# Performance work log

Measured on AMD Instinct MI355X. Metric: run time of the kernel, lower is better.

The kernel has to match this reference:

```python
import jax, jax.numpy as jnp
import numpy as np

B, N, C = 4096, 20, 512
S_VIEWS = 8
N_VIEWS = 20


def setup_inputs() -> dict:
    key = jax.random.key(0)
    k1, k2, k3, k4 = jax.random.split(key, 4)
    F0 = jax.random.normal(k1, (B, N, C), dtype=jnp.float32)
    vertices0 = jax.random.normal(k2, (B, N, 3), dtype=jnp.float32)
    W1 = jax.random.normal(k3, (C, 256), dtype=jnp.float32) * 0.04
    b1 = jnp.zeros((256,), dtype=jnp.float32)
    W2 = jax.random.normal(k4, (256, 40), dtype=jnp.float32) * 0.06
    b2 = jnp.zeros((40,), dtype=jnp.float32)
    return {"F0": F0, "vertices0": vertices0, "W1": W1, "b1": b1, "W2": W2, "b2": b2, "k": 8}


def _cls(x, W1, b1, W2, b2):
    # Linear(512,256) -> LeakyReLU(0.2) -> Linear(256,40)
    h = x @ W1 + b1
    h = jnp.where(h > 0, h, 0.2 * h)
    return h @ W2 + b2


def reference(F0, vertices0, W1, b1, W2, b2, k):
    # F0: [B, N, C]; vertices0: [B, N, 3]
    pooled_F = jnp.sum(F0, axis=1) / N_VIEWS                 # [B, C]
    pred = jnp.argmax(_cls(pooled_F, W1, b1, W2, b2), -1)    # [B] predicted class per sample
    score = _cls(F0, W1, b1, W2, b2)                         # [B, N, 40]
    # score[arange(B), :, pred] -> per-view score of the predicted class
    score_F = jnp.take_along_axis(score, pred[:, None, None], axis=2)[..., 0]  # [B, N]
    _, idx = jax.lax.top_k(score_F, S_VIEWS)                 # [B, S]
    F_new = jnp.take_along_axis(F0, idx[:, :, None], axis=1)            # [B, S, C]
    vertices_new = jnp.take_along_axis(vertices0, idx[:, :, None], axis=1)  # [B, S, 3]
    return (F_new, score, vertices_new)
```

## Files before the change

kernel.cpp:

```cpp
#include <hip/hip_runtime.h>
#include <cstdint>

#define BB 4096
#define NV 20
#define CC 512
#define HH 256
#define NC 40
#define SV 8
#define GG 3
#define TAU 2e-4f

typedef short short8 __attribute__((ext_vector_type(8)));
typedef float f32x4 __attribute__((ext_vector_type(4)));
typedef unsigned short ushort4v __attribute__((ext_vector_type(4)));

__device__ __forceinline__ unsigned short f2bf(float x) {
    unsigned u = __float_as_uint(x);
    unsigned r = (u + 0x7FFFu + ((u >> 16) & 1u)) >> 16;
    return (unsigned short)r;
}
__device__ __forceinline__ float bf2f(unsigned short h) {
    return __uint_as_float(((unsigned)h) << 16);
}

#define MFMA16(A, B, C) __builtin_amdgcn_mfma_f32_16x16x32_bf16(A, B, C, 0, 0, 0)
#define BC8(x) __builtin_bit_cast(short8, x)

__global__ void w1pack_kernel(const float* __restrict__ W1,
                              unsigned short* __restrict__ w1fh,
                              unsigned short* __restrict__ w1fl) {
    int e = blockIdx.x * 256 + threadIdx.x;
    int j3 = e & 7, kq = (e >> 3) & 3, n = (e >> 5) & 255, ks = e >> 13;
    int k = ks * 32 + kq * 8 + j3;
    float x = W1[k * HH + n];
    unsigned short h = f2bf(x);
    w1fh[e] = h;
    w1fl[e] = f2bf(x - bf2f(h));
}

__global__ void w2pack_kernel(const float* __restrict__ W2,
                              unsigned short* __restrict__ w2fh,
                              unsigned short* __restrict__ w2fl) {
    int e = blockIdx.x * 256 + threadIdx.x;
    int j3 = e & 7, kq = (e >> 3) & 3;
    int t = e >> 5;
    int n = t % 48, ks = t / 48;
    int k = ks * 32 + kq * 8 + j3;
    float x = (n < NC) ? W2[k * NC + n] : 0.f;
    unsigned short h = f2bf(x);
    w2fh[e] = h;
    w2fl[e] = f2bf(x - bf2f(h));
}

__global__ __launch_bounds__(256, 3) void fused_kernel(
    const float* __restrict__ F0, const float* __restrict__ V0,
    const float* __restrict__ W1, const float* __restrict__ b1,
    const float* __restrict__ W2, const float* __restrict__ b2,
    const unsigned short* __restrict__ w1fh, const unsigned short* __restrict__ w1fl,
    const unsigned short* __restrict__ w2fh, const unsigned short* __restrict__ w2fl,
    float* __restrict__ outF, float* __restrict__ outS, float* __restrict__ outV)
{
    const int blk = blockIdx.x;
    const int j = threadIdx.x;
    const int L = j & 63, wq = j >> 6, l15 = L & 15, kq = L >> 4;

    __shared__ __align__(16) char lds[51040];
    __shared__ int idx8[GG][SV];
    __shared__ int flags0[GG], flags1[GG], predS[GG];
    __shared__ double part[NV][4];
    __shared__ double SFdS[NV];

    unsigned short* Ahi0 = (unsigned short*)lds;
    unsigned short* Alo0 = Ahi0 + 64 * 72;
    unsigned short* Ahi1 = (unsigned short*)(lds + 18432);
    unsigned short* Alo1 = Ahi1 + 64 * 72;
    unsigned short* Hhi  = (unsigned short*)lds;
    unsigned short* Hlo  = Hhi + 32 * 264;
    float*  Sc      = (float*)(lds + 40960);
    double* pooledD = (double*)lds;
    double* Dbuf    = (double*)(lds + 4096);
    double* Sd      = (double*)(lds + 6144);
    float*  Xf      = (float*)lds;

    f32x4 acc[4][4];
#pragma unroll
    for (int mt = 0; mt < 4; ++mt)
#pragma unroll
        for (int nt = 0; nt < 4; ++nt) acc[mt][nt] = (f32x4){0.f, 0.f, 0.f, 0.f};

    const float4* srcp[4];
    int ldst[4];
    bool sval[4];
#pragma unroll
    for (int i = 0; i < 4; ++i) {
        int f = j + 256 * i;
        int row = f >> 4, k4 = f & 15;
        sval[i] = (row < 60);
        int bi = (row >= 40) ? 2 : (row >= 20) ? 1 : 0;
        int r = row - 20 * bi;
        int batch = blk * GG + bi; if (batch > BB - 1) batch = BB - 1;
        srcp[i] = (const float4*)(F0 + ((size_t)batch * NV + r) * CC) + k4;
        ldst[i] = row * 72 + k4 * 4;
    }

    float4 rv[4];
    auto STAGE_LOAD = [&](int kc) {
#pragma unroll
        for (int i = 0; i < 4; ++i)
            if (sval[i]) rv[i] = srcp[i][kc * 16];
    };
    auto STAGE_CONVERT = [&](unsigned short* __restrict__ Ah,
                             unsigned short* __restrict__ Al) {
#pragma unroll
        for (int i = 0; i < 4; ++i) {
            ushort4v hv = {0, 0, 0, 0}, lv = {0, 0, 0, 0};
            if (sval[i]) {
                float4 x = rv[i];
                hv.x = f2bf(x.x); lv.x = f2bf(x.x - bf2f(hv.x));
                hv.y = f2bf(x.y); lv.y = f2bf(x.y - bf2f(hv.y));
                hv.z = f2bf(x.z); lv.z = f2bf(x.z - bf2f(hv.z));
                hv.w = f2bf(x.w); lv.w = f2bf(x.w - bf2f(hv.w));
            }
            *(ushort4v*)&Ah[ldst[i]] = hv;
            *(ushort4v*)&Al[ldst[i]] = lv;
        }
    };

    const uint4* Bh = (const uint4*)w1fh;
    const uint4* Bl = (const uint4*)w1fl;

    STAGE_LOAD(0);
    STAGE_CONVERT(Ahi0, Alo0);
    STAGE_LOAD(1);
    __syncthreads();

    unsigned short *Ahc = Ahi0, *Alc = Alo0, *Ahn = Ahi1, *Aln = Alo1;
    for (int kc = 0; kc < 8; ++kc) {
        if (kc < 7) {
            STAGE_CONVERT(Ahn, Aln);
            if (kc < 6) STAGE_LOAD(kc + 2);
        }
#pragma unroll
        for (int ks_l = 0; ks_l < 2; ++ks_l) {
            int ks = kc * 2 + ks_l;
            uint4 bh[4], bl[4];
#pragma unroll
            for (int nt = 0; nt < 4; ++nt) {
                int bi1 = (ks * 256 + wq * 64 + nt * 16 + l15) * 4 + kq;
                bh[nt] = Bh[bi1]; bl[nt] = Bl[bi1];
            }
#pragma unroll
            for (int mt = 0; mt < 4; ++mt) {
                int off = (mt * 16 + l15) * 72 + ks_l * 32 + kq * 8;
                short8 Ah = BC8(*(const uint4*)&Ahc[off]);
                short8 Al = BC8(*(const uint4*)&Alc[off]);
#pragma unroll
                for (int nt = 0; nt < 4; ++nt) {
                    short8 Bhv = BC8(bh[nt]), Blv = BC8(bl[nt]);
                    acc[mt][nt] = MFMA16(Ah, Bhv, acc[mt][nt]);
                    acc[mt][nt] = MFMA16(Ah, Blv, acc[mt][nt]);
                    acc[mt][nt] = MFMA16(Al, Bhv, acc[mt][nt]);
                }
            }
        }
        __syncthreads();
        unsigned short* t;
        t = Ahc; Ahc = Ahn; Ahn = t;
        t = Alc; Alc = Aln; Aln = t;
    }

    const uint4* B2h = (const uint4*)w2fh;
    const uint4* B2l = (const uint4*)w2fl;
#pragma unroll
    for (int p = 0; p < 2; ++p) {
        __syncthreads();
#pragma unroll
        for (int mt2 = 0; mt2 < 2; ++mt2) {
            int mt = 2 * p + mt2;
            bool skip = (p == 1 && mt2 == 1 && kq == 3);
#pragma unroll
            for (int nt = 0; nt < 4; ++nt) {
                int col = wq * 64 + nt * 16 + l15;
                float bc = b1[col];
#pragma unroll
                for (int reg = 0; reg < 4; ++reg) {
                    int hb = mt2 * 16 + kq * 4 + reg;
                    float h = acc[mt][nt][reg] + bc;
                    h = (h > 0.f) ? h : 0.2f * h;
                    if (!skip) {
                        unsigned short hh = f2bf(h);
                        Hhi[hb * 264 + col] = hh;
                        Hlo[hb * 264 + col] = f2bf(h - bf2f(hh));
                    }
                }
            }
        }
        if (p == 1) {
#pragma unroll
            for (int nt = 0; nt < 4; ++nt) {
                int col = wq * 64 + nt * 16 + l15;
                float p0 = 0.f, p1 = 0.f, p2 = 0.f;
#pragma unroll
                for (int mt = 0; mt < 4; ++mt)
#pragma unroll
                    for (int reg = 0; reg < 4; ++reg) {
                        int g = mt * 16 + kq * 4 + reg;
                        float v = acc[mt][nt][reg];
                        p0 += (g < 20) ? v : 0.f;
                        p1 += (g >= 20 && g < 40) ? v : 0.f;
                        p2 += (g >= 40 && g < 60) ? v : 0.f;
                    }
                p0 += __shfl_xor(p0, 16); p0 += __shfl_xor(p0, 32);
                p1 += __shfl_xor(p1, 16); p1 += __shfl_xor(p1, 32);
                p2 += __shfl_xor(p2, 16); p2 += __shfl_xor(p2, 32);
                if (kq < 3) {
                    float s = (kq == 0) ? p0 : (kq == 1) ? p1 : p2;
                    float h = s * (1.0f / NV) + b1[col];
                    h = (h > 0.f) ? h : 0.2f * h;
                    unsigned short hh = f2bf(h);
                    Hhi[(28 + kq) * 264 + col] = hh;
                    Hlo[(28 + kq) * 264 + col] = f2bf(h - bf2f(hh));
                } else {
                    Hhi[31 * 264 + col] = 0;
                    Hlo[31 * 264 + col] = 0;
                }
            }
        }
        __syncthreads();

        if (wq < 3) {
            f32x4 sacc[2];
            sacc[0] = (f32x4){0.f, 0.f, 0.f, 0.f};
            sacc[1] = (f32x4){0.f, 0.f, 0.f, 0.f};
            for (int ks2 = 0; ks2 < 8; ++ks2) {
                int bi2 = (ks2 * 48 + wq * 16 + l15) * 4 + kq;
                short8 Bhv = BC8(B2h[bi2]), Blv = BC8(B2l[bi2]);
#pragma unroll
                for (int tt = 0; tt < 2; ++tt) {
                    int off = (tt * 16 + l15) * 264 + ks2 * 32 + kq * 8;
                    short8 Ah2 = BC8(*(const uint4*)&Hhi[off]);
                    short8 Al2 = BC8(*(const uint4*)&Hlo[off]);
                    sacc[tt] = MFMA16(Ah2, Bhv, sacc[tt]);
                    sacc[tt] = MFMA16(Ah2, Blv, sacc[tt]);
                    sacc[tt] = MFMA16(Al2, Bhv, sacc[tt]);
                }
            }
            int cls = wq * 16 + l15;
            if (cls < NC) {
                float bc2 = b2[cls];
#pragma unroll
                for (int tt = 0; tt < 2; ++tt)
#pragma unroll
                    for (int reg = 0; reg < 4; ++reg) {
                        int lm = 32 * p + tt * 16 + kq * 4 + reg;
                        float sv = sacc[tt][reg] + bc2;
                        if (lm < 60) {
                            int bi = (lm >= 40) ? 2 : (lm >= 20) ? 1 : 0;
                            int r = lm - 20 * bi;
                            Sc[bi * 840 + r * NC + cls] = sv;
                        } else if (lm < 63) {
                            Sc[(lm - 60) * 840 + NV * NC + cls] = sv;
                        }
                    }
            }
        }
    }
    __syncthreads();

    if (j < GG) {
        const float* sp = &Sc[j * 840 + NV * NC];
        int p = 0;
        float m1 = sp[0];
        for (int c = 1; c < NC; ++c)
            if (sp[c] > m1) { m1 = sp[c]; p = c; }
        float m2 = -1e30f;
        for (int c = 0; c < NC; ++c)
            if (c != p && sp[c] > m2) m2 = sp[c];
        flags0[j] = (m1 - m2 < TAU) ? 1 : 0;
        predS[j] = p;
    }
    __syncthreads();

    for (int bi = 0; bi < GG; ++bi) {
        if (flags0[bi]) {
            int batch = blk * GG + bi; if (batch > BB - 1) batch = BB - 1;
            const float* Xb = F0 + (size_t)batch * (NV * CC);
            for (int c = j; c < CC; c += 256) {
                double s = 0.0;
                for (int r = 0; r < NV; ++r) s += (double)Xb[r * CC + c];
                pooledD[c] = s / (double)NV;
            }
            __syncthreads();
            double a = 0.0;
            for (int c = 0; c < CC; ++c) a += pooledD[c] * (double)W1[c * HH + j];
            double h = a + (double)b1[j];
            h = (h > 0.0) ? h : 0.2 * h;
            Dbuf[j] = h;
            __syncthreads();
            if (j < NC) {
                double s = 0.0;
                for (int k = 0; k < HH; ++k) s += Dbuf[k] * (double)W2[k * NC + j];
                Sd[j] = s + (double)b2[j];
            }
            __syncthreads();
            if (j == 0) {
                int p = 0;
                double m = Sd[0];
                for (int c = 1; c < NC; ++c)
                    if (Sd[c] > m) { m = Sd[c]; p = c; }
                predS[bi] = p;
            }
            __syncthreads();
        }
    }

    if (j < GG) {
        int p = predS[j];
        float v[NV];
#pragma unroll
        for (int n = 0; n < NV; ++n) v[n] = Sc[j * 840 + n * NC + p];
        int ord[9];
        float vals[9];
        unsigned taken = 0;
#pragma unroll
        for (int s = 0; s < 9; ++s) {
            int bi = 0;
            float bv = -1e30f;
#pragma unroll
            for (int n = 0; n < NV; ++n)
                if (!((taken >> n) & 1u) && v[n] > bv) { bv = v[n]; bi = n; }
            taken |= 1u << bi;
            ord[s] = bi;
            vals[s] = bv;
        }
        int fix = 0;
#pragma unroll
        for (int s = 0; s < 8; ++s)
            if (vals[s] - vals[s + 1] < TAU) fix = 1;
        flags1[j] = fix;
        if (!fix)
#pragma unroll
            for (int s = 0; s < SV; ++s) idx8[j][s] = ord[s];
    }
    __syncthreads();

    for (int bi = 0; bi < GG; ++bi) {
        if (flags1[bi]) {
            int batch = blk * GG + bi; if (batch > BB - 1) batch = BB - 1;
            const float* Xb = F0 + (size_t)batch * (NV * CC);
            int p = predS[bi];
            for (int t = j; t < NV * CC / 4; t += 256)
                ((float4*)Xf)[t] = ((const float4*)Xb)[t];
            __syncthreads();
            const double b1d = (double)b1[j];
            const double w2jp = (double)W2[j * NC + p];
#pragma unroll
            for (int half = 0; half < 2; ++half) {
                double a[10];
#pragma unroll
                for (int r = 0; r < 10; ++r) a[r] = 0.0;
                for (int c = 0; c < CC; c += 4) {
                    double w0 = (double)W1[(c + 0) * HH + j];
                    double w1v = (double)W1[(c + 1) * HH + j];
                    double w2v = (double)W1[(c + 2) * HH + j];
                    double w3v = (double)W1[(c + 3) * HH + j];
#pragma unroll
                    for (int r = 0; r < 10; ++r) {
                        const float4 x = *(const float4*)&Xf[(half * 10 + r) * CC + c];
                        a[r] += (double)x.x * w0;
                        a[r] += (double)x.y * w1v;
                        a[r] += (double)x.z * w2v;
                        a[r] += (double)x.w * w3v;
                    }
                }
#pragma unroll
                for (int r = 0; r < 10; ++r) {
                    double h = a[r] + b1d;
                    h = (h > 0.0) ? h : 0.2 * h;
                    double val = h * w2jp;
#pragma unroll
                    for (int off = 32; off >= 1; off >>= 1)
                        val += __shfl_xor(val, off);
                    if (L == 0) part[half * 10 + r][wq] = val;
                }
            }
            __syncthreads();
            if (j < NV)
                SFdS[j] = part[j][0] + part[j][1] + part[j][2] + part[j][3]
                        + (double)b2[p];
            __syncthreads();
            if (j == 0) {
                unsigned taken = 0;
                for (int s = 0; s < SV; ++s) {
                    int bsel = 0;
                    double bv = -1e300;
                    for (int n = 0; n < NV; ++n)
                        if (!((taken >> n) & 1u) && SFdS[n] > bv) { bv = SFdS[n]; bsel = n; }
                    taken |= 1u << bsel;
                    idx8[bi][s] = bsel;
                }
            }
            __syncthreads();
        }
    }

    for (int t = j; t < GG * NV * NC; t += 256) {
        int bi = t / 800, o = t - bi * 800;
        int batch = blk * GG + bi; if (batch > BB - 1) batch = BB - 1;
        outS[(size_t)batch * (NV * NC) + o] = Sc[bi * 840 + o];
    }

    for (int t = j; t < GG * SV * (CC / 4); t += 256) {
        int bi = t >> 10;
        int s = (t >> 7) & 7;
        int t4 = t & 127;
        int batch = blk * GG + bi; if (batch > BB - 1) batch = BB - 1;
        int row = idx8[bi][s];
        const float4* src = (const float4*)(F0 + ((size_t)batch * NV + row) * CC);
        float4* dst = (float4*)(outF + ((size_t)batch * SV + s) * CC);
        dst[t4] = src[t4];
    }

    if (j < GG * SV * 3) {
        int bi = j / 24, o = j - bi * 24;
        int s = o / 3, d = o - s * 3;
        int batch = blk * GG + bi; if (batch > BB - 1) batch = BB - 1;
        outV[((size_t)batch * SV + s) * 3 + d] =
            V0[((size_t)batch * NV + idx8[bi][s]) * 3 + d];
    }
}

extern "C" void kernel_launch(void* const* d_in, const int* in_sizes, int n_in,
                              void* d_out, int out_size, void* d_ws, size_t ws_size,
                              hipStream_t stream) {
    const float* F0 = (const float*)d_in[0];
    const float* V0 = (const float*)d_in[1];
    const float* W1 = (const float*)d_in[2];
    const float* b1 = (const float*)d_in[3];
    const float* W2 = (const float*)d_in[4];
    const float* b2 = (const float*)d_in[5];

    char* ws = (char*)d_ws;
    unsigned short* w1fh = (unsigned short*)ws;
    unsigned short* w1fl = (unsigned short*)(ws + 262144);
    unsigned short* w2fh = (unsigned short*)(ws + 524288);
    unsigned short* w2fl = (unsigned short*)(ws + 548864);

    float* out = (float*)d_out;
    float* outF = out;
    float* outS = out + (size_t)BB * SV * CC;
    float* outV = outS + (size_t)BB * NV * NC;

    w1pack_kernel<<<512, 256, 0, stream>>>(W1, w1fh, w1fl);
    w2pack_kernel<<<48, 256, 0, stream>>>(W2, w2fh, w2fl);
    fused_kernel<<<(BB + GG - 1) / GG, 256, 0, stream>>>(
        F0, V0, W1, b1, W2, b2, w1fh, w1fl, w2fh, w2fl, outF, outS, outV);
}
```

Measured before the change: 443.1 us.

## Move near-tie fp64 fallback into a separate rescue kernel

```diff
diff --git a/kernel.cpp b/kernel.cpp
--- a/kernel.cpp
+++ b/kernel.cpp
@@ -58,17 +58,15 @@
     const float* __restrict__ W2, const float* __restrict__ b2,
     const unsigned short* __restrict__ w1fh, const unsigned short* __restrict__ w1fl,
     const unsigned short* __restrict__ w2fh, const unsigned short* __restrict__ w2fl,
+    int* __restrict__ rflag, int* __restrict__ rpred,
     float* __restrict__ outF, float* __restrict__ outS, float* __restrict__ outV)
 {
     const int blk = blockIdx.x;
     const int j = threadIdx.x;
     const int L = j & 63, wq = j >> 6, l15 = L & 15, kq = L >> 4;
 
-    __shared__ __align__(16) char lds[51040];
+    __shared__ __align__(16) char lds[46944];
     __shared__ int idx8[GG][SV];
-    __shared__ int flags0[GG], flags1[GG], predS[GG];
-    __shared__ double part[NV][4];
-    __shared__ double SFdS[NV];
 
     unsigned short* Ahi0 = (unsigned short*)lds;
     unsigned short* Alo0 = Ahi0 + 64 * 72;
@@ -76,11 +74,7 @@
     unsigned short* Alo1 = Ahi1 + 64 * 72;
     unsigned short* Hhi  = (unsigned short*)lds;
     unsigned short* Hlo  = Hhi + 32 * 264;
-    float*  Sc      = (float*)(lds + 40960);
-    double* pooledD = (double*)lds;
-    double* Dbuf    = (double*)(lds + 4096);
-    double* Sd      = (double*)(lds + 6144);
-    float*  Xf      = (float*)lds;
+    float*  Sc      = (float*)(lds + 36864);
 
     f32x4 acc[4][4];
 #pragma unroll
@@ -276,46 +270,8 @@
         float m2 = -1e30f;
         for (int c = 0; c < NC; ++c)
             if (c != p && sp[c] > m2) m2 = sp[c];
-        flags0[j] = (m1 - m2 < TAU) ? 1 : 0;
-        predS[j] = p;
-    }
-    __syncthreads();
-
-    for (int bi = 0; bi < GG; ++bi) {
-        if (flags0[bi]) {
-            int batch = blk * GG + bi; if (batch > BB - 1) batch = BB - 1;
-            const float* Xb = F0 + (size_t)batch * (NV * CC);
-            for (int c = j; c < CC; c += 256) {
-                double s = 0.0;
-                for (int r = 0; r < NV; ++r) s += (double)Xb[r * CC + c];
-                pooledD[c] = s / (double)NV;
-            }
-            __syncthreads();
-            double a = 0.0;
-            for (int c = 0; c < CC; ++c) a += pooledD[c] * (double)W1[c * HH + j];
-            double h = a + (double)b1[j];
-            h = (h > 0.0) ? h : 0.2 * h;
-            Dbuf[j] = h;
-            __syncthreads();
-            if (j < NC) {
-                double s = 0.0;
-                for (int k = 0; k < HH; ++k) s += Dbuf[k] * (double)W2[k * NC + j];
-                Sd[j] = s + (double)b2[j];
-            }
-            __syncthreads();
-            if (j == 0) {
-                int p = 0;
-                double m = Sd[0];
-                for (int c = 1; c < NC; ++c)
-                    if (Sd[c] > m) { m = Sd[c]; p = c; }
-                predS[bi] = p;
-            }
-            __syncthreads();
-        }
-    }
-
-    if (j < GG) {
-        int p = predS[j];
+        int f0 = (m1 - m2 < TAU) ? 1 : 0;
+
         float v[NV];
 #pragma unroll
         for (int n = 0; n < NV; ++n) v[n] = Sc[j * 840 + n * NC + p];
@@ -337,72 +293,14 @@
 #pragma unroll
         for (int s = 0; s < 8; ++s)
             if (vals[s] - vals[s + 1] < TAU) fix = 1;
-        flags1[j] = fix;
-        if (!fix)
-#pragma unroll
-            for (int s = 0; s < SV; ++s) idx8[j][s] = ord[s];
-    }
-    __syncthreads();
-
-    for (int bi = 0; bi < GG; ++bi) {
-        if (flags1[bi]) {
-            int batch = blk * GG + bi; if (batch > BB - 1) batch = BB - 1;
-            const float* Xb = F0 + (size_t)batch * (NV * CC);
-            int p = predS[bi];
-            for (int t = j; t < NV * CC / 4; t += 256)
-                ((float4*)Xf)[t] = ((const float4*)Xb)[t];
-            __syncthreads();
-            const double b1d = (double)b1[j];
-            const double w2jp = (double)W2[j * NC + p];
-#pragma unroll
-            for (int half = 0; half < 2; ++half) {
-                double a[10];
-#pragma unroll
-                for (int r = 0; r < 10; ++r) a[r] = 0.0;
-                for (int c = 0; c < CC; c += 4) {
-                    double w0 = (double)W1[(c + 0) * HH + j];
-                    double w1v = (double)W1[(c + 1) * HH + j];
-                    double w2v = (double)W1[(c + 2) * HH + j];
-                    double w3v = (double)W1[(c + 3) * HH + j];
-#pragma unroll
-                    for (int r = 0; r < 10; ++r) {
-                        const float4 x = *(const float4*)&Xf[(half * 10 + r) * CC + c];
-                        a[r] += (double)x.x * w0;
-                        a[r] += (double)x.y * w1v;
-                        a[r] += (double)x.z * w2v;
-                        a[r] += (double)x.w * w3v;
-                    }
-                }
-#pragma unroll
-                for (int r = 0; r < 10; ++r) {
-                    double h = a[r] + b1d;
-                    h = (h > 0.0) ? h : 0.2 * h;
-                    double val = h * w2jp;
-#pragma unroll
-                    for (int off = 32; off >= 1; off >>= 1)
-                        val += __shfl_xor(val, off);
-                    if (L == 0) part[half * 10 + r][wq] = val;
-                }
-            }
-            __syncthreads();
-            if (j < NV)
-                SFdS[j] = part[j][0] + part[j][1] + part[j][2] + part[j][3]
-                        + (double)b2[p];
-            __syncthreads();
-            if (j == 0) {
-                unsigned taken = 0;
-                for (int s = 0; s < SV; ++s) {
-                    int bsel = 0;
-                    double bv = -1e300;
-                    for (int n = 0; n < NV; ++n)
-                        if (!((taken >> n) & 1u) && SFdS[n] > bv) { bv = SFdS[n]; bsel = n; }
-                    taken |= 1u << bsel;
-                    idx8[bi][s] = bsel;
-                }
-            }
-            __syncthreads();
-        }
-    }
+#pragma unroll
+        for (int s = 0; s < SV; ++s) idx8[j][s] = ord[s];
+
+        int batch = blk * GG + j; if (batch > BB - 1) batch = BB - 1;
+        rflag[batch] = f0 ? 1 : (fix ? 2 : 0);
+        rpred[batch] = p;
+    }
+    __syncthreads();
 
     for (int t = j; t < GG * NV * NC; t += 256) {
         int bi = t / 800, o = t - bi * 800;
@@ -430,6 +328,130 @@
     }
 }
 
+__global__ __launch_bounds__(256) void rescue_kernel(
+    const float* __restrict__ F0, const float* __restrict__ V0,
+    const float* __restrict__ W1, const float* __restrict__ b1,
+    const float* __restrict__ W2, const float* __restrict__ b2,
+    const int* __restrict__ rflag, const int* __restrict__ rpred,
+    float* __restrict__ outF, float* __restrict__ outV)
+{
+    const int b = blockIdx.x;
+    const int flag = rflag[b];
+    if (flag == 0) return;
+
+    const int j = threadIdx.x;
+    const int L = j & 63, wq = j >> 6;
+
+    __shared__ __align__(16) float Xf[NV * CC];
+    __shared__ double pooledD[CC];
+    __shared__ double Dbuf[HH];
+    __shared__ double Sd[NC];
+    __shared__ double part[NV][4];
+    __shared__ double SFdS[NV];
+    __shared__ int predSh;
+    __shared__ int idxs[SV];
+
+    const float* Xb = F0 + (size_t)b * (NV * CC);
+    for (int t = j; t < NV * CC / 4; t += 256)
+        ((float4*)Xf)[t] = ((const float4*)Xb)[t];
+    __syncthreads();
+
+    if (flag == 1) {
+        for (int c = j; c < CC; c += 256) {
+            double s = 0.0;
+            for (int r = 0; r < NV; ++r) s += (double)Xf[r * CC + c];
+            pooledD[c] = s / (double)NV;
+        }
+        __syncthreads();
+        double a = 0.0;
+        for (int c = 0; c < CC; ++c) a += pooledD[c] * (double)W1[c * HH + j];
+        double h = a + (double)b1[j];
+        h = (h > 0.0) ? h : 0.2 * h;
+        Dbuf[j] = h;
+        __syncthreads();
+        if (j < NC) {
+            double s = 0.0;
+            for (int k = 0; k < HH; ++k) s += Dbuf[k] * (double)W2[k * NC + j];
+            Sd[j] = s + (double)b2[j];
+        }
+        __syncthreads();
+        if (j == 0) {
+            int p = 0;
+            double m = Sd[0];
+            for (int c = 1; c < NC; ++c)
+                if (Sd[c] > m) { m = Sd[c]; p = c; }
+            predSh = p;
+        }
+        __syncthreads();
+    } else {
+        if (j == 0) predSh = rpred[b];
+        __syncthreads();
+    }
+    const int p = predSh;
+
+    const double b1d = (double)b1[j];
+    const double w2jp = (double)W2[j * NC + p];
+#pragma unroll
+    for (int half = 0; half < 2; ++half) {
+        double a[10];
+#pragma unroll
+        for (int r = 0; r < 10; ++r) a[r] = 0.0;
+        for (int c = 0; c < CC; c += 4) {
+            double w0 = (double)W1[(c + 0) * HH + j];
+            double w1v = (double)W1[(c + 1) * HH + j];
+            double w2v = (double)W1[(c + 2) * HH + j];
+            double w3v = (double)W1[(c + 3) * HH + j];
+#pragma unroll
+            for (int r = 0; r < 10; ++r) {
+                const float4 x = *(const float4*)&Xf[(half * 10 + r) * CC + c];
+                a[r] += (double)x.x * w0;
+                a[r] += (double)x.y * w1v;
+                a[r] += (double)x.z * w2v;
+                a[r] += (double)x.w * w3v;
+            }
+        }
+#pragma unroll
+        for (int r = 0; r < 10; ++r) {
+            double h = a[r] + b1d;
+            h = (h > 0.0) ? h : 0.2 * h;
+            double val = h * w2jp;
+#pragma unroll
+            for (int off = 32; off >= 1; off >>= 1)
+                val += __shfl_xor(val, off);
+            if (L == 0) part[half * 10 + r][wq] = val;
+        }
+    }
+    __syncthreads();
+    if (j < NV)
+        SFdS[j] = part[j][0] + part[j][1] + part[j][2] + part[j][3]
+                + (double)b2[p];
+    __syncthreads();
+    if (j == 0) {
+        unsigned taken = 0;
+        for (int s = 0; s < SV; ++s) {
+            int bsel = 0;
+            double bv = -1e300;
+            for (int n = 0; n < NV; ++n)
+                if (!((taken >> n) & 1u) && SFdS[n] > bv) { bv = SFdS[n]; bsel = n; }
+            taken |= 1u << bsel;
+            idxs[s] = bsel;
+        }
+    }
+    __syncthreads();
+
+    for (int t = j; t < SV * (CC / 4); t += 256) {
+        int s = t >> 7, t4 = t & 127;
+        int row = idxs[s];
+        ((float4*)(outF + ((size_t)b * SV + s) * CC))[t4] =
+            ((const float4*)(F0 + ((size_t)b * NV + row) * CC))[t4];
+    }
+    if (j < SV * 3) {
+        int s = j / 3, d = j - s * 3;
+        outV[((size_t)b * SV + s) * 3 + d] =
+            V0[((size_t)b * NV + idxs[s]) * 3 + d];
+    }
+}
+
 extern "C" void kernel_launch(void* const* d_in, const int* in_sizes, int n_in,
                               void* d_out, int out_size, void* d_ws, size_t ws_size,
                               hipStream_t stream) {
@@ -445,6 +467,8 @@
     unsigned short* w1fl = (unsigned short*)(ws + 262144);
     unsigned short* w2fh = (unsigned short*)(ws + 524288);
     unsigned short* w2fl = (unsigned short*)(ws + 548864);
+    int* rflag = (int*)(ws + 573440);
+    int* rpred = (int*)(ws + 589824);
 
     float* out = (float*)d_out;
     float* outF = out;
@@ -454,5 +478,8 @@
     w1pack_kernel<<<512, 256, 0, stream>>>(W1, w1fh, w1fl);
     w2pack_kernel<<<48, 256, 0, stream>>>(W2, w2fh, w2fl);
     fused_kernel<<<(BB + GG - 1) / GG, 256, 0, stream>>>(
-        F0, V0, W1, b1, W2, b2, w1fh, w1fl, w2fh, w2fl, outF, outS, outV);
-}
+        F0, V0, W1, b1, W2, b2, w1fh, w1fl, w2fh, w2fl, rflag, rpred,
+        outF, outS, outV);
+    rescue_kernel<<<BB, 256, 0, stream>>>(
+        F0, V0, W1, b1, W2, b2, rflag, rpred, outF, outV);
+}
```

Result: slower. 464.8 us (+4.9%).
